# Optimization experiments

Hardware: AMD Instinct MI355X
Metric: run time of the kernel (lower is better)

Reference implementation:

```python
import jax, jax.numpy as jnp
import numpy as np

B, C, H, W = 2, 128, 64, 64
D_STATE, D_CONV, EXPAND = 16, 4, 2
D_INNER = EXPAND * C
DT_RANK = (C + 15) // 16  # ceil(d_model/16) = 8


def layernorm(x, w, b):
    # WithBias_LayerNorm over last (channel) dim, unbiased=False variance
    mu = jnp.mean(x, axis=-1, keepdims=True)
    var = jnp.mean((x - mu) ** 2, axis=-1, keepdims=True)
    return (x - mu) / jnp.sqrt(var + 1e-5) * w + b


def causal_conv1d_silu(x, w, b):
    # x: (b, d, l); w: (d, k) depthwise; causal pad k-1 on left, then SiLU
    k = w.shape[1]
    out = jax.lax.conv_general_dilated(
        x, w[:, None, :], window_strides=(1,), padding=[(k - 1, 0)],
        dimension_numbers=('NCH', 'OIH', 'NCH'), feature_group_count=w.shape[0])
    return jax.nn.silu(out + b[:, None])


def selective_scan(dA, dBu, Cm):
    # dA, dBu: (b, d, l, n); Cm: (b, n, l) -> y: (b, d, l)
    dA_t = jnp.moveaxis(dA, 2, 0)    # (l, b, d, n)
    dBu_t = jnp.moveaxis(dBu, 2, 0)  # (l, b, d, n)
    C_t = jnp.moveaxis(Cm, 2, 0)     # (l, b, n)

    def step(h, inp):
        a, bu, c = inp
        h = a * h + bu
        y = jnp.einsum('bdn,bn->bd', h, c)
        return h, y

    h0 = jnp.zeros(dA.shape[:2] + (dA.shape[3],), dA.dtype)
    _, ys = jax.lax.scan(step, h0, (dA_t, dBu_t, C_t))
    return jnp.moveaxis(ys, 0, 2)  # (b, d, l)


def mamba_branch(x3, W_in, W_z, conv_w, conv_b, W_x, W_dt, b_dt, A, D, W_out):
    # x3: (b, l, d_model) normalized input
    x = jnp.einsum('bld,ed->bel', x3, W_in)  # (b, d_inner, l)
    z = jnp.einsum('bld,ed->bel', x3, W_z)
    x = causal_conv1d_silu(x, conv_w, conv_b)
    xdbl = jnp.einsum('bdl,ed->bel', x, W_x)  # (b, dt_rank+2n, l)
    dt_low = xdbl[:, :DT_RANK]
    Bm = xdbl[:, DT_RANK:DT_RANK + D_STATE]
    Cm = xdbl[:, DT_RANK + D_STATE:]
    delta = jax.nn.softplus(jnp.einsum('brl,dr->bdl', dt_low, W_dt) + b_dt[:, None])
    dA = jnp.exp(delta[:, :, :, None] * A[None, :, None, :])           # (b,d,l,n)
    dBu = jnp.einsum('bdl,bnl->bdln', delta * x, Bm)                    # (b,d,l,n)
    y = selective_scan(dA, dBu, Cm)
    y = y + D[:, None] * x
    y = y * jax.nn.silu(z)
    return jnp.einsum('bdl,od->blo', y, W_out)  # (b, l, d_model)


def setup_inputs() -> dict:
    key = jax.random.key(0)
    ks = jax.random.split(key, 24)
    rn = lambda k, shp, s: jax.random.normal(k, shp, dtype=jnp.float32) * s
    inp = {}
    inp['pan'] = rn(ks[0], (B, C, H, W), 1.0)
    inp['ms'] = rn(ks[1], (B, C, H, W), 1.0)
    inp['norm_w_pan'] = jnp.ones((C,), jnp.float32)
    inp['norm_b_pan'] = jnp.zeros((C,), jnp.float32)
    inp['norm_w_ms'] = jnp.ones((C,), jnp.float32)
    inp['norm_b_ms'] = jnp.zeros((C,), jnp.float32)
    inp['W_in_pan'] = rn(ks[2], (D_INNER, C), C ** -0.5)
    inp['W_in_ms'] = rn(ks[3], (D_INNER, C), C ** -0.5)
    inp['W_z_pan'] = rn(ks[4], (D_INNER, C), C ** -0.5)
    inp['W_z_ms'] = rn(ks[5], (D_INNER, C), C ** -0.5)
    inp['conv_w_pan'] = rn(ks[6], (D_INNER, D_CONV), D_CONV ** -0.5)
    inp['conv_b_pan'] = rn(ks[7], (D_INNER,), 0.02)
    inp['conv_w_ms'] = rn(ks[8], (D_INNER, D_CONV), D_CONV ** -0.5)
    inp['conv_b_ms'] = rn(ks[9], (D_INNER,), 0.02)
    inp['W_x_pan'] = rn(ks[10], (DT_RANK + 2 * D_STATE, D_INNER), D_INNER ** -0.5)
    inp['W_x_ms'] = rn(ks[11], (DT_RANK + 2 * D_STATE, D_INNER), D_INNER ** -0.5)
    dt_std = DT_RANK ** -0.5
    inp['W_dt_pan'] = jax.random.uniform(ks[12], (D_INNER, DT_RANK), jnp.float32, -dt_std, dt_std)
    inp['W_dt_ms'] = jax.random.uniform(ks[13], (D_INNER, DT_RANK), jnp.float32, -dt_std, dt_std)
    # dt bias init: inverse-softplus of dt ~ logU[1e-3, 1e-1]
    u = np.asarray(jax.random.uniform(ks[14], (D_INNER,)))
    dt = np.exp(u * (np.log(0.1) - np.log(0.001)) + np.log(0.001)).clip(min=1e-4)
    inv_dt = dt + np.log(-np.expm1(-dt))
    inp['b_dt_pan'] = jnp.asarray(inv_dt, jnp.float32)
    inp['b_dt_ms'] = jnp.asarray(inv_dt, jnp.float32)
    inp['A_log'] = jnp.log(jnp.broadcast_to(jnp.arange(1, D_STATE + 1, dtype=jnp.float32), (D_INNER, D_STATE)))
    inp['D_pan'] = jnp.ones((D_INNER,), jnp.float32)
    inp['D_ms'] = jnp.ones((D_INNER,), jnp.float32)
    inp['W_out_pan'] = rn(ks[15], (C, D_INNER), D_INNER ** -0.5)
    inp['W_out_ms'] = rn(ks[16], (C, D_INNER), D_INNER ** -0.5)
    return inp


def reference(pan, ms, norm_w_pan, norm_b_pan, norm_w_ms, norm_b_ms,
              W_in_pan, W_in_ms, W_z_pan, W_z_ms,
              conv_w_pan, conv_b_pan, conv_w_ms, conv_b_ms,
              W_x_pan, W_x_ms, W_dt_pan, W_dt_ms, b_dt_pan, b_dt_ms,
              A_log, D_pan, D_ms, W_out_pan, W_out_ms):
    b, c, h, w = pan.shape
    A = -jnp.exp(A_log)
    pan3 = layernorm(pan.reshape(b, c, h * w).transpose(0, 2, 1), norm_w_pan, norm_b_pan)
    ms3 = layernorm(ms.reshape(b, c, h * w).transpose(0, 2, 1), norm_w_ms, norm_b_ms)
    out_pan = mamba_branch(pan3, W_in_pan, W_z_pan, conv_w_pan, conv_b_pan,
                           W_x_pan, W_dt_pan, b_dt_pan, A, D_pan, W_out_pan)
    out_ms = mamba_branch(ms3, W_in_ms, W_z_ms, conv_w_ms, conv_b_ms,
                          W_x_ms, W_dt_ms, b_dt_ms, A, D_ms, W_out_ms)
    out_pan = out_pan.transpose(0, 2, 1).reshape(b, c, h, w)
    out_ms = out_ms.transpose(0, 2, 1).reshape(b, c, h, w)
    return (out_pan, out_ms)
```

## Files before the change

kernel.cpp:

```cpp
#include <hip/hip_runtime.h>
#include <hip/hip_bf16.h>

constexpr int BB = 2;
constexpr int CC = 128;
constexpr int LL = 4096;
constexpr int DI = 256;
constexpr int DS = 16;
constexpr int DR = 8;
constexpr int DX = 40;
constexpr int NZ = 2 * BB;
constexpr int CH = 8;
constexpr int NCH = LL / CH;
constexpr int SEG = 32;

typedef short bf16x8 __attribute__((ext_vector_type(8)));
typedef float f32x4 __attribute__((ext_vector_type(4)));

__device__ __forceinline__ unsigned short f2bf(float x) {
    __hip_bfloat16 h = __float2bfloat16(x);
    return *(unsigned short*)&h;
}
__device__ __forceinline__ float bflo(unsigned u) { return __uint_as_float(u << 16); }
__device__ __forceinline__ float bfhi(unsigned u) { return __uint_as_float(u & 0xffff0000u); }
__device__ __forceinline__ float fast_rcp(float x) { return __builtin_amdgcn_rcpf(x); }
__device__ __forceinline__ float siluf(float x) { return x * fast_rcp(1.f + __expf(-x)); }
__device__ __forceinline__ float softplusf(float x) {
    const float z = exp2f(x * 1.44269504f);
    return (x > 20.f) ? x : 0.69314718f * log2f(1.f + z);
}

__global__ __launch_bounds__(256) void convert_w_kernel(
    const float* __restrict__ Winp, const float* __restrict__ Winm,
    const float* __restrict__ Wzp, const float* __restrict__ Wzm,
    const float* __restrict__ Woutp, const float* __restrict__ Woutm,
    const float* __restrict__ Wxp, const float* __restrict__ Wxm,
    unsigned short* __restrict__ dst)
{
    const int i = blockIdx.x * 256 + threadIdx.x;
    const float* src; int off;
    if (i < 32768)       { src = Winp;  off = i; }
    else if (i < 65536)  { src = Winm;  off = i - 32768; }
    else if (i < 98304)  { src = Wzp;   off = i - 65536; }
    else if (i < 131072) { src = Wzm;   off = i - 98304; }
    else if (i < 163840) { src = Woutp; off = i - 131072; }
    else if (i < 196608) { src = Woutm; off = i - 163840; }
    else if (i < 206848) { src = Wxp;   off = i - 196608; }
    else                 { src = Wxm;   off = i - 206848; }
    dst[i] = f2bf(src[off]);
}

__global__ __launch_bounds__(256) void layernorm_kernel(
    const float* __restrict__ pan, const float* __restrict__ ms,
    const float* __restrict__ wpan, const float* __restrict__ bpan,
    const float* __restrict__ wms, const float* __restrict__ bms,
    unsigned short* __restrict__ x3b)
{
    const int zi = blockIdx.y;
    const int br = zi >> 1, b = zi & 1;
    const float* inp = br ? ms : pan;
    const float* wp = br ? wms : wpan;
    const float* bp = br ? bms : bpan;
    const int l0 = blockIdx.x * 64;
    const int t = threadIdx.x;
    const int lo = t & 63, c4 = t >> 6;
    const float* base = inp + (size_t)b * CC * LL + l0 + lo;
    float vals[32];
    float s = 0.f, s2 = 0.f;
    #pragma unroll
    for (int i = 0; i < 32; i++) {
        const int c = c4 * 32 + i;
        const float v = base[(size_t)c * LL];
        vals[i] = v; s += v; s2 += v * v;
    }
    __shared__ float red[2][4][64];
    red[0][c4][lo] = s; red[1][c4][lo] = s2;
    __syncthreads();
    const float S  = red[0][0][lo] + red[0][1][lo] + red[0][2][lo] + red[0][3][lo];
    const float S2 = red[1][0][lo] + red[1][1][lo] + red[1][2][lo] + red[1][3][lo];
    const float mu = S * (1.f / CC);
    const float var = S2 * (1.f / CC) - mu * mu;
    const float rstd = rsqrtf(var + 1e-5f);
    unsigned short* out = x3b + (size_t)zi * CC * LL + l0 + lo;
    #pragma unroll
    for (int i = 0; i < 32; i++) {
        const int c = c4 * 32 + i;
        out[(size_t)c * LL] = f2bf((vals[i] - mu) * rstd * wp[c] + bp[c]);
    }
}

__global__ __launch_bounds__(256) void gemm_inz_mfma(
    const unsigned short* __restrict__ wb, const unsigned short* __restrict__ x3b,
    float* __restrict__ xpre, unsigned short* __restrict__ zb16)
{
    const int zi = blockIdx.z;
    const int my = blockIdx.y;
    const unsigned short* W = wb + (my >= 4 ? 65536 : 0) + (zi >= BB ? 32768 : 0);
    const int mbase = (my & 3) * 64;
    const unsigned short* Xb = x3b + (size_t)zi * CC * LL;
    const int n0 = blockIdx.x * 64;
    const int t = threadIdx.x;
    const int w = t >> 6, ln = t & 63;
    const int nf = ln & 15, qb = ln >> 4;
    bf16x8 afrag[4];
    const int mrow = mbase + w * 16 + nf;
    #pragma unroll
    for (int c = 0; c < 4; c++)
        afrag[c] = *(const bf16x8*)(W + (size_t)mrow * CC + c * 32 + qb * 8);
    __shared__ unsigned short Bs[64][40];
    unsigned* Bw = (unsigned*)Bs;
    f32x4 acc[4] = {};
    const int kp = t >> 4, n4 = (t & 15) * 4;
    #pragma unroll
    for (int kc = 0; kc < 4; kc++) {
        const ushort4 a0 = *(const ushort4*)(Xb + (size_t)(kc * 32 + 2 * kp) * LL + n0 + n4);
        const ushort4 a1 = *(const ushort4*)(Xb + (size_t)(kc * 32 + 2 * kp + 1) * LL + n0 + n4);
        if (kc) __syncthreads();
        Bw[(n4 + 0) * 20 + kp] = (unsigned)a0.x | ((unsigned)a1.x << 16);
        Bw[(n4 + 1) * 20 + kp] = (unsigned)a0.y | ((unsigned)a1.y << 16);
        Bw[(n4 + 2) * 20 + kp] = (unsigned)a0.z | ((unsigned)a1.z << 16);
        Bw[(n4 + 3) * 20 + kp] = (unsigned)a0.w | ((unsigned)a1.w << 16);
        __syncthreads();
        #pragma unroll
        for (int ns = 0; ns < 4; ns++) {
            const bf16x8 bf = *(const bf16x8*)(&Bs[ns * 16 + nf][qb * 8]);
            acc[ns] = __builtin_amdgcn_mfma_f32_16x16x32_bf16(afrag[kc], bf, acc[ns], 0, 0, 0);
        }
    }
    if (my >= 4) {
        #pragma unroll
        for (int ns = 0; ns < 4; ns++)
            #pragma unroll
            for (int r = 0; r < 4; r++) {
                const int m = mbase + w * 16 + qb * 4 + r;
                zb16[((size_t)zi * DI + m) * LL + n0 + ns * 16 + nf] = f2bf(acc[ns][r]);
            }
    } else {
        #pragma unroll
        for (int ns = 0; ns < 4; ns++)
            #pragma unroll
            for (int r = 0; r < 4; r++) {
                const int m = mbase + w * 16 + qb * 4 + r;
                xpre[((size_t)zi * DI + m) * LL + n0 + ns * 16 + nf] = acc[ns][r];
            }
    }
}

__global__ __launch_bounds__(256) void conv_silu_kernel(
    const float* __restrict__ xpre,
    const float* __restrict__ cw0, const float* __restrict__ cb0,
    const float* __restrict__ cw1, const float* __restrict__ cb1,
    unsigned short* __restrict__ xc)
{
    const int idx = blockIdx.x * 256 + threadIdx.x;
    const int row = idx >> 9;
    const int l0 = (idx & 511) * CH;
    const int zi = row >> 8, d = row & (DI - 1);
    const float* cw = (zi >= BB) ? cw1 : cw0;
    const float* cb = (zi >= BB) ? cb1 : cb0;
    const float w0 = cw[d * 4 + 0], w1 = cw[d * 4 + 1];
    const float w2 = cw[d * 4 + 2], w3 = cw[d * 4 + 3];
    const float bias = cb[d];
    const float* x_g = xpre + (size_t)row * LL;
    float xv[CH + 3];
    if (l0 > 0) {
        const float4 hm = *(const float4*)(x_g + l0 - 4);
        xv[0] = hm.y; xv[1] = hm.z; xv[2] = hm.w;
    } else { xv[0] = 0.f; xv[1] = 0.f; xv[2] = 0.f; }
    #pragma unroll
    for (int j = 0; j < 2; j++) {
        const float4 v = *(const float4*)(x_g + l0 + 4 * j);
        xv[4 * j + 3] = v.x; xv[4 * j + 4] = v.y;
        xv[4 * j + 5] = v.z; xv[4 * j + 6] = v.w;
    }
    ushort4 r0, r1;
    #pragma unroll
    for (int i = 0; i < CH; i++) {
        const float val = siluf(w0 * xv[i] + w1 * xv[i + 1] + w2 * xv[i + 2] + w3 * xv[i + 3] + bias);
        if (i < 4) ((unsigned short*)&r0)[i] = f2bf(val);
        else       ((unsigned short*)&r1)[i - 4] = f2bf(val);
    }
    unsigned short* out = xc + (size_t)row * LL + l0;
    *(ushort4*)(out + 0) = r0;
    *(ushort4*)(out + 4) = r1;
}

__global__ __launch_bounds__(256) void gemm_x_mfma(
    const unsigned short* __restrict__ wb, const unsigned short* __restrict__ xc,
    unsigned short* __restrict__ xdbl16)
{
    const int zi = blockIdx.z;
    const unsigned short* W = wb + 196608 + (zi >= BB ? 10240 : 0);
    const unsigned short* Xb = xc + (size_t)zi * DI * LL;
    const int n0 = blockIdx.x * 64;
    const int t = threadIdx.x;
    const int w = t >> 6, ln = t & 63;
    const int nf = ln & 15, qb = ln >> 4;
    bf16x8 zfrag;
    #pragma unroll
    for (int j = 0; j < 8; j++) zfrag[j] = 0;
    bf16x8 afrag[8];
    const int mrow = w * 16 + nf;
    #pragma unroll
    for (int c = 0; c < 8; c++)
        afrag[c] = (mrow < DX) ? *(const bf16x8*)(W + (size_t)mrow * DI + c * 32 + qb * 8) : zfrag;
    __shared__ unsigned short Bs[64][40];
    unsigned* Bw = (unsigned*)Bs;
    f32x4 acc[4] = {};
    const int kp = t >> 4, n4 = (t & 15) * 4;
    #pragma unroll
    for (int kc = 0; kc < 8; kc++) {
        const ushort4 a0 = *(const ushort4*)(Xb + (size_t)(kc * 32 + 2 * kp) * LL + n0 + n4);
        const ushort4 a1 = *(const ushort4*)(Xb + (size_t)(kc * 32 + 2 * kp + 1) * LL + n0 + n4);
        if (kc) __syncthreads();
        Bw[(n4 + 0) * 20 + kp] = (unsigned)a0.x | ((unsigned)a1.x << 16);
        Bw[(n4 + 1) * 20 + kp] = (unsigned)a0.y | ((unsigned)a1.y << 16);
        Bw[(n4 + 2) * 20 + kp] = (unsigned)a0.z | ((unsigned)a1.z << 16);
        Bw[(n4 + 3) * 20 + kp] = (unsigned)a0.w | ((unsigned)a1.w << 16);
        __syncthreads();
        #pragma unroll
        for (int ns = 0; ns < 4; ns++) {
            const bf16x8 bf = *(const bf16x8*)(&Bs[ns * 16 + nf][qb * 8]);
            acc[ns] = __builtin_amdgcn_mfma_f32_16x16x32_bf16(afrag[kc], bf, acc[ns], 0, 0, 0);
        }
    }
    #pragma unroll
    for (int ns = 0; ns < 4; ns++)
        #pragma unroll
        for (int r = 0; r < 4; r++) {
            const int m = w * 16 + qb * 4 + r;
            if (m < DX)
                xdbl16[((size_t)zi * DX + m) * LL + n0 + ns * 16 + nf] = f2bf(acc[ns][r]);
        }
}

__global__ __launch_bounds__(256) void gemm_out_mfma(
    const unsigned short* __restrict__ wb, const unsigned short* __restrict__ yb,
    float* __restrict__ outg)
{
    const int zi = blockIdx.z;
    const unsigned short* W = wb + 131072 + (zi >= BB ? 32768 : 0);
    const int mbase = blockIdx.y * 64;
    const unsigned short* Xb = yb + (size_t)zi * DI * LL;
    const int n0 = blockIdx.x * 64;
    const int t = threadIdx.x;
    const int w = t >> 6, ln = t & 63;
    const int nf = ln & 15, qb = ln >> 4;
    bf16x8 afrag[8];
    const int mrow = mbase + w * 16 + nf;
    #pragma unroll
    for (int c = 0; c < 8; c++)
        afrag[c] = *(const bf16x8*)(W + (size_t)mrow * DI + c * 32 + qb * 8);
    __shared__ unsigned short Bs[64][40];
    unsigned* Bw = (unsigned*)Bs;
    f32x4 acc[4] = {};
    const int kp = t >> 4, n4 = (t & 15) * 4;
    #pragma unroll
    for (int kc = 0; kc < 8; kc++) {
        const ushort4 a0 = *(const ushort4*)(Xb + (size_t)(kc * 32 + 2 * kp) * LL + n0 + n4);
        const ushort4 a1 = *(const ushort4*)(Xb + (size_t)(kc * 32 + 2 * kp + 1) * LL + n0 + n4);
        if (kc) __syncthreads();
        Bw[(n4 + 0) * 20 + kp] = (unsigned)a0.x | ((unsigned)a1.x << 16);
        Bw[(n4 + 1) * 20 + kp] = (unsigned)a0.y | ((unsigned)a1.y << 16);
        Bw[(n4 + 2) * 20 + kp] = (unsigned)a0.z | ((unsigned)a1.z << 16);
        Bw[(n4 + 3) * 20 + kp] = (unsigned)a0.w | ((unsigned)a1.w << 16);
        __syncthreads();
        #pragma unroll
        for (int ns = 0; ns < 4; ns++) {
            const bf16x8 bf = *(const bf16x8*)(&Bs[ns * 16 + nf][qb * 8]);
            acc[ns] = __builtin_amdgcn_mfma_f32_16x16x32_bf16(afrag[kc], bf, acc[ns], 0, 0, 0);
        }
    }
    #pragma unroll
    for (int ns = 0; ns < 4; ns++)
        #pragma unroll
        for (int r = 0; r < 4; r++) {
            const int m = mbase + w * 16 + qb * 4 + r;
            outg[((size_t)zi * CC + m) * LL + n0 + ns * 16 + nf] = acc[ns][r];
        }
}

__global__ __launch_bounds__(512, 8) void scan_fused(
    const unsigned short* __restrict__ xc, const unsigned short* __restrict__ xdbl16,
    const float* __restrict__ A_log,
    const float* __restrict__ Wdt0, const float* __restrict__ Wdt1,
    const float* __restrict__ bdt0, const float* __restrict__ bdt1,
    const float* __restrict__ D0, const float* __restrict__ D1,
    const unsigned short* __restrict__ zb16, unsigned short* __restrict__ yb)
{
    const int blk = blockIdx.x;
    const int zi = blk >> 8;
    const int d  = blk & (DI - 1);
    const int t = threadIdx.x;
    const int l0 = t * CH;
    __shared__ float Ssh[DS * (NCH + 1)];
    __shared__ float sdl_sh[NCH];
    __shared__ float Pseg[DS * (SEG + 1)];
    __shared__ float Sseg[DS * (SEG + 1)];
    const unsigned short* xdb = xdbl16 + (size_t)zi * DX * LL;
    const float* Wdt = (zi >= BB) ? Wdt1 : Wdt0;
    const float* bdt = (zi >= BB) ? bdt1 : bdt0;
    const float dbias = bdt[d];
    float rx[CH];
    {
        const uint4 xv4 = *(const uint4*)(xc + (size_t)blk * LL + l0);
        rx[0] = bflo(xv4.x); rx[1] = bfhi(xv4.x);
        rx[2] = bflo(xv4.y); rx[3] = bfhi(xv4.y);
        rx[4] = bflo(xv4.z); rx[5] = bfhi(xv4.z);
        rx[6] = bflo(xv4.w); rx[7] = bfhi(xv4.w);
    }
    float e[CH], rdlx[CH];
    {
        float acc[CH];
        #pragma unroll
        for (int i = 0; i < CH; i++) acc[i] = dbias;
        #pragma unroll
        for (int r = 0; r < DR; r++) {
            const float wr = Wdt[d * DR + r];
            const uint4 v = *(const uint4*)(xdb + (size_t)r * LL + l0);
            acc[0] = fmaf(wr, bflo(v.x), acc[0]); acc[1] = fmaf(wr, bfhi(v.x), acc[1]);
            acc[2] = fmaf(wr, bflo(v.y), acc[2]); acc[3] = fmaf(wr, bfhi(v.y), acc[3]);
            acc[4] = fmaf(wr, bflo(v.z), acc[4]); acc[5] = fmaf(wr, bfhi(v.z), acc[5]);
            acc[6] = fmaf(wr, bflo(v.w), acc[6]); acc[7] = fmaf(wr, bfhi(v.w), acc[7]);
        }
        float sdl = 0.f;
        #pragma unroll
        for (int i = 0; i < CH; i++) {
            const float sp = softplusf(acc[i]);
            sdl += sp;
            rdlx[i] = sp * rx[i];
            e[i] = __expf(-sp);
        }
        sdl_sh[t] = sdl;
    }
    bool fast = true;
    #pragma unroll
    for (int n = 0; n < DS; n++)
        fast = fast && (fabsf(__expf(A_log[d * DS + n]) - (float)(n + 1)) < 1e-3f);
    const unsigned short* Bbase = xdb + (size_t)DR * LL;
    const unsigned short* Cbase = Bbase + (size_t)DS * LL;
    float y[CH];
    const int n2 = t & 15, sg = t >> 4;

    if (fast) {
        float pw[CH];
        #pragma unroll
        for (int i = 0; i < CH; i++) pw[i] = 1.f;
        #pragma unroll 2
        for (int n = 0; n < DS; n++) {
            const uint4 bv = *(const uint4*)(Bbase + (size_t)n * LL + l0);
            float hn = 0.f;
            pw[0] *= e[0]; hn = fmaf(pw[0], hn, rdlx[0] * bflo(bv.x));
            pw[1] *= e[1]; hn = fmaf(pw[1], hn, rdlx[1] * bfhi(bv.x));
            pw[2] *= e[2]; hn = fmaf(pw[2], hn, rdlx[2] * bflo(bv.y));
            pw[3] *= e[3]; hn = fmaf(pw[3], hn, rdlx[3] * bfhi(bv.y));
            pw[4] *= e[4]; hn = fmaf(pw[4], hn, rdlx[4] * bflo(bv.z));
            pw[5] *= e[5]; hn = fmaf(pw[5], hn, rdlx[5] * bfhi(bv.z));
            pw[6] *= e[6]; hn = fmaf(pw[6], hn, rdlx[6] * bflo(bv.w));
            pw[7] *= e[7]; hn = fmaf(pw[7], hn, rdlx[7] * bfhi(bv.w));
            Ssh[n * (NCH + 1) + t] = hn;
        }
        __syncthreads();
        {
            const float Ann = -(float)(n2 + 1);
            float P = 1.f, S = 0.f;
            #pragma unroll
            for (int k = 0; k < 16; k++) {
                const int c = sg * 16 + k;
                const float p = __expf(Ann * sdl_sh[c]);
                const float s = Ssh[n2 * (NCH + 1) + c];
                S = fmaf(p, S, s);
                P *= p;
            }
            Pseg[n2 * (SEG + 1) + sg] = P;
            Sseg[n2 * (SEG + 1) + sg] = S;
        }
        __syncthreads();
        if (t < DS) {
            float h = 0.f;
            #pragma unroll 4
            for (int c2 = 0; c2 < SEG; c2++) {
                const float p = Pseg[t * (SEG + 1) + c2];
                const float s = Sseg[t * (SEG + 1) + c2];
                Sseg[t * (SEG + 1) + c2] = h;
                h = fmaf(p, h, s);
            }
        }
        __syncthreads();
        {
            const float Ann = -(float)(n2 + 1);
            float h = Sseg[n2 * (SEG + 1) + sg];
            #pragma unroll
            for (int k = 0; k < 16; k++) {
                const int c = sg * 16 + k;
                const float p = __expf(Ann * sdl_sh[c]);
                const float s = Ssh[n2 * (NCH + 1) + c];
                Ssh[n2 * (NCH + 1) + c] = h;
                h = fmaf(p, h, s);
            }
        }
        __syncthreads();
        #pragma unroll
        for (int i = 0; i < CH; i++) { y[i] = 0.f; pw[i] = 1.f; }
        #pragma unroll 2
        for (int n = 0; n < DS; n++) {
            const uint4 bv = *(const uint4*)(Bbase + (size_t)n * LL + l0);
            const uint4 cv = *(const uint4*)(Cbase + (size_t)n * LL + l0);
            float hn = Ssh[n * (NCH + 1) + t];
            pw[0] *= e[0]; hn = fmaf(pw[0], hn, rdlx[0] * bflo(bv.x)); y[0] = fmaf(hn, bflo(cv.x), y[0]);
            pw[1] *= e[1]; hn = fmaf(pw[1], hn, rdlx[1] * bfhi(bv.x)); y[1] = fmaf(hn, bfhi(cv.x), y[1]);
            pw[2] *= e[2]; hn = fmaf(pw[2], hn, rdlx[2] * bflo(bv.y)); y[2] = fmaf(hn, bflo(cv.y), y[2]);
            pw[3] *= e[3]; hn = fmaf(pw[3], hn, rdlx[3] * bfhi(bv.y)); y[3] = fmaf(hn, bfhi(cv.y), y[3]);
            pw[4] *= e[4]; hn = fmaf(pw[4], hn, rdlx[4] * bflo(bv.z)); y[4] = fmaf(hn, bflo(cv.z), y[4]);
            pw[5] *= e[5]; hn = fmaf(pw[5], hn, rdlx[5] * bfhi(bv.z)); y[5] = fmaf(hn, bfhi(cv.z), y[5]);
            pw[6] *= e[6]; hn = fmaf(pw[6], hn, rdlx[6] * bflo(bv.w)); y[6] = fmaf(hn, bflo(cv.w), y[6]);
            pw[7] *= e[7]; hn = fmaf(pw[7], hn, rdlx[7] * bfhi(bv.w)); y[7] = fmaf(hn, bfhi(cv.w), y[7]);
        }
    } else {
        float rdl[CH];
        #pragma unroll
        for (int i = 0; i < CH; i++) rdl[i] = -0.69314718f * log2f(e[i]);
        #pragma unroll 2
        for (int n = 0; n < DS; n++) {
            const float An = -__expf(A_log[d * DS + n]);
            const uint4 bv = *(const uint4*)(Bbase + (size_t)n * LL + l0);
            float hn = 0.f;
            hn = fmaf(__expf(rdl[0] * An), hn, rdlx[0] * bflo(bv.x));
            hn = fmaf(__expf(rdl[1] * An), hn, rdlx[1] * bfhi(bv.x));
            hn = fmaf(__expf(rdl[2] * An), hn, rdlx[2] * bflo(bv.y));
            hn = fmaf(__expf(rdl[3] * An), hn, rdlx[3] * bfhi(bv.y));
            hn = fmaf(__expf(rdl[4] * An), hn, rdlx[4] * bflo(bv.z));
            hn = fmaf(__expf(rdl[5] * An), hn, rdlx[5] * bfhi(bv.z));
            hn = fmaf(__expf(rdl[6] * An), hn, rdlx[6] * bflo(bv.w));
            hn = fmaf(__expf(rdl[7] * An), hn, rdlx[7] * bfhi(bv.w));
            Ssh[n * (NCH + 1) + t] = hn;
        }
        __syncthreads();
        {
            const float Ann = -__expf(A_log[d * DS + n2]);
            float P = 1.f, S = 0.f;
            #pragma unroll
            for (int k = 0; k < 16; k++) {
                const int c = sg * 16 + k;
                const float p = __expf(Ann * sdl_sh[c]);
                const float s = Ssh[n2 * (NCH + 1) + c];
                S = fmaf(p, S, s);
                P *= p;
            }
            Pseg[n2 * (SEG + 1) + sg] = P;
            Sseg[n2 * (SEG + 1) + sg] = S;
        }
        __syncthreads();
        if (t < DS) {
            float h = 0.f;
            #pragma unroll 4
            for (int c2 = 0; c2 < SEG; c2++) {
                const float p = Pseg[t * (SEG + 1) + c2];
                const float s = Sseg[t * (SEG + 1) + c2];
                Sseg[t * (SEG + 1) + c2] = h;
                h = fmaf(p, h, s);
            }
        }
        __syncthreads();
        {
            const float Ann = -__expf(A_log[d * DS + n2]);
            float h = Sseg[n2 * (SEG + 1) + sg];
            #pragma unroll
            for (int k = 0; k < 16; k++) {
                const int c = sg * 16 + k;
                const float p = __expf(Ann * sdl_sh[c]);
                const float s = Ssh[n2 * (NCH + 1) + c];
                Ssh[n2 * (NCH + 1) + c] = h;
                h = fmaf(p, h, s);
            }
        }
        __syncthreads();
        #pragma unroll
        for (int i = 0; i < CH; i++) y[i] = 0.f;
        #pragma unroll 2
        for (int n = 0; n < DS; n++) {
            const float An = -__expf(A_log[d * DS + n]);
            const uint4 bv = *(const uint4*)(Bbase + (size_t)n * LL + l0);
            const uint4 cv = *(const uint4*)(Cbase + (size_t)n * LL + l0);
            float hn = Ssh[n * (NCH + 1) + t];
            hn = fmaf(__expf(rdl[0] * An), hn, rdlx[0] * bflo(bv.x)); y[0] = fmaf(hn, bflo(cv.x), y[0]);
            hn = fmaf(__expf(rdl[1] * An), hn, rdlx[1] * bfhi(bv.x)); y[1] = fmaf(hn, bfhi(cv.x), y[1]);
            hn = fmaf(__expf(rdl[2] * An), hn, rdlx[2] * bflo(bv.y)); y[2] = fmaf(hn, bflo(cv.y), y[2]);
            hn = fmaf(__expf(rdl[3] * An), hn, rdlx[3] * bfhi(bv.y)); y[3] = fmaf(hn, bfhi(cv.y), y[3]);
            hn = fmaf(__expf(rdl[4] * An), hn, rdlx[4] * bflo(cv.z)); y[4] = fmaf(hn, bflo(cv.z), y[4]);
            hn = fmaf(__expf(rdl[5] * An), hn, rdlx[5] * bfhi(bv.z)); y[5] = fmaf(hn, bfhi(cv.z), y[5]);
            hn = fmaf(__expf(rdl[6] * An), hn, rdlx[6] * bflo(bv.w)); y[6] = fmaf(hn, bflo(cv.w), y[6]);
            hn = fmaf(__expf(rdl[7] * An), hn, rdlx[7] * bfhi(bv.w)); y[7] = fmaf(hn, bfhi(cv.w), y[7]);
        }
    }
    const float Dd = ((zi >= BB) ? D1 : D0)[d];
    const unsigned short* z_g = zb16 + (size_t)blk * LL + l0;
    unsigned short* y_g = yb + (size_t)blk * LL + l0;
    {
        const uint4 zv = *(const uint4*)z_g;
        float zf[CH];
        zf[0] = bflo(zv.x); zf[1] = bfhi(zv.x); zf[2] = bflo(zv.y); zf[3] = bfhi(zv.y);
        zf[4] = bflo(zv.z); zf[5] = bfhi(zv.z); zf[6] = bflo(zv.w); zf[7] = bfhi(zv.w);
        ushort4 r0, r1;
        #pragma unroll
        for (int i = 0; i < CH; i++) {
            const float val = (y[i] + Dd * rx[i]) * siluf(zf[i]);
            if (i < 4) ((unsigned short*)&r0)[i] = f2bf(val);
            else       ((unsigned short*)&r1)[i - 4] = f2bf(val);
        }
        *(ushort4*)(y_g + 0) = r0;
        *(ushort4*)(y_g + 4) = r1;
    }
}

extern "C" void kernel_launch(void* const* d_in, const int* in_sizes, int n_in,
                              void* d_out, int out_size, void* d_ws, size_t ws_size,
                              hipStream_t stream)
{
    (void)in_sizes; (void)n_in; (void)out_size; (void)ws_size;
    auto fp = [&](int i) { return (const float*)d_in[i]; };
    const float *pan = fp(0), *ms = fp(1);
    const float *nwp = fp(2), *nbp = fp(3), *nwm = fp(4), *nbm = fp(5);
    const float *Winp = fp(6), *Winm = fp(7), *Wzp = fp(8), *Wzm = fp(9);
    const float *cwp = fp(10), *cbp = fp(11), *cwm = fp(12), *cbm = fp(13);
    const float *Wxp = fp(14), *Wxm = fp(15);
    const float *Wdtp = fp(16), *Wdtm = fp(17), *bdtp = fp(18), *bdtm = fp(19);
    const float *Alog = fp(20), *Dp = fp(21), *Dm = fp(22);
    const float *Woutp = fp(23), *Woutm = fp(24);

    float* ws = (float*)d_ws;
    unsigned short* x3b = (unsigned short*)ws;
    float* xpre = ws + (size_t)NZ * CC * LL / 2;
    unsigned short* zb16 = (unsigned short*)(xpre + (size_t)NZ * DI * LL);
    unsigned short* xdbl16 = zb16 + (size_t)NZ * DI * LL;
    unsigned short* yb = xdbl16 + (size_t)NZ * DX * LL;
    unsigned short* wb = yb + (size_t)NZ * DI * LL;
    unsigned short* xc = wb + 217088;
    float* out = (float*)d_out;

    convert_w_kernel<<<dim3(848), 256, 0, stream>>>(Winp, Winm, Wzp, Wzm, Woutp, Woutm, Wxp, Wxm, wb);
    layernorm_kernel<<<dim3(LL / 64, NZ), 256, 0, stream>>>(pan, ms, nwp, nbp, nwm, nbm, x3b);
    gemm_inz_mfma<<<dim3(LL / 64, 8, NZ), 256, 0, stream>>>(wb, x3b, xpre, zb16);
    conv_silu_kernel<<<dim3(NZ * DI * (LL / CH) / 256), 256, 0, stream>>>(xpre, cwp, cbp, cwm, cbm, xc);
    gemm_x_mfma<<<dim3(LL / 64, 1, NZ), 256, 0, stream>>>(wb, xc, xdbl16);
    scan_fused<<<dim3(NZ * DI), 512, 0, stream>>>(xc, xdbl16, Alog, Wdtp, Wdtm, bdtp, bdtm,
                                                  Dp, Dm, zb16, yb);
    gemm_out_mfma<<<dim3(LL / 64, 2, NZ), 256, 0, stream>>>(wb, yb, out);
}
```

Measured before the change: 172.2 us.

## Fuse layernorm with weight conversion and conv+SiLU into x-projection GEMM

Merges the weight-conversion and layernorm kernels into one launch and folds the causal depthwise conv plus SiLU into the x-projection GEMM's operand staging. The in-projection result is now stored as bf16 instead of fp32, halving that intermediate's traffic and dropping a separate conv kernel pass. It also raises the unroll in a scan loop and fixes a wrong operand (cv.z instead of bv.z) in the scan recurrence. The bf16 intermediate adds rounding before the conv, and the fused GEMM reloads neighbouring elements for the conv halo.

```diff
diff --git a/kernel.cpp b/kernel.cpp
--- a/kernel.cpp
+++ b/kernel.cpp
@@ -22,6 +22,7 @@
 }
 __device__ __forceinline__ float bflo(unsigned u) { return __uint_as_float(u << 16); }
 __device__ __forceinline__ float bfhi(unsigned u) { return __uint_as_float(u & 0xffff0000u); }
+__device__ __forceinline__ float bfu(unsigned short u) { return __uint_as_float((unsigned)u << 16); }
 __device__ __forceinline__ float fast_rcp(float x) { return __builtin_amdgcn_rcpf(x); }
 __device__ __forceinline__ float siluf(float x) { return x * fast_rcp(1.f + __expf(-x)); }
 __device__ __forceinline__ float softplusf(float x) {
@@ -29,39 +30,38 @@
     return (x > 20.f) ? x : 0.69314718f * log2f(1.f + z);
 }
 
-__global__ __launch_bounds__(256) void convert_w_kernel(
+__global__ __launch_bounds__(256) void prep_kernel(
+    const float* __restrict__ pan, const float* __restrict__ ms,
+    const float* __restrict__ wpan, const float* __restrict__ bpan,
+    const float* __restrict__ wms, const float* __restrict__ bms,
     const float* __restrict__ Winp, const float* __restrict__ Winm,
     const float* __restrict__ Wzp, const float* __restrict__ Wzm,
     const float* __restrict__ Woutp, const float* __restrict__ Woutm,
     const float* __restrict__ Wxp, const float* __restrict__ Wxm,
-    unsigned short* __restrict__ dst)
+    unsigned short* __restrict__ x3b, unsigned short* __restrict__ wb)
 {
-    const int i = blockIdx.x * 256 + threadIdx.x;
-    const float* src; int off;
-    if (i < 32768)       { src = Winp;  off = i; }
-    else if (i < 65536)  { src = Winm;  off = i - 32768; }
-    else if (i < 98304)  { src = Wzp;   off = i - 65536; }
-    else if (i < 131072) { src = Wzm;   off = i - 98304; }
-    else if (i < 163840) { src = Woutp; off = i - 131072; }
-    else if (i < 196608) { src = Woutm; off = i - 163840; }
-    else if (i < 206848) { src = Wxp;   off = i - 196608; }
-    else                 { src = Wxm;   off = i - 206848; }
-    dst[i] = f2bf(src[off]);
-}
-
-__global__ __launch_bounds__(256) void layernorm_kernel(
-    const float* __restrict__ pan, const float* __restrict__ ms,
-    const float* __restrict__ wpan, const float* __restrict__ bpan,
-    const float* __restrict__ wms, const float* __restrict__ bms,
-    unsigned short* __restrict__ x3b)
-{
-    const int zi = blockIdx.y;
+    const int bx = blockIdx.x;
+    const int t = threadIdx.x;
+    if (bx >= 256) {
+        const int i = (bx - 256) * 256 + t;
+        const float* src; int off;
+        if (i < 32768)       { src = Winp;  off = i; }
+        else if (i < 65536)  { src = Winm;  off = i - 32768; }
+        else if (i < 98304)  { src = Wzp;   off = i - 65536; }
+        else if (i < 131072) { src = Wzm;   off = i - 98304; }
+        else if (i < 163840) { src = Woutp; off = i - 131072; }
+        else if (i < 196608) { src = Woutm; off = i - 163840; }
+        else if (i < 206848) { src = Wxp;   off = i - 196608; }
+        else                 { src = Wxm;   off = i - 206848; }
+        wb[i] = f2bf(src[off]);
+        return;
+    }
+    const int zi = bx >> 6;
     const int br = zi >> 1, b = zi & 1;
     const float* inp = br ? ms : pan;
     const float* wp = br ? wms : wpan;
     const float* bp = br ? bms : bpan;
-    const int l0 = blockIdx.x * 64;
-    const int t = threadIdx.x;
+    const int l0 = (bx & 63) * 64;
     const int lo = t & 63, c4 = t >> 6;
     const float* base = inp + (size_t)b * CC * LL + l0 + lo;
     float vals[32];
@@ -90,7 +90,7 @@
 
 __global__ __launch_bounds__(256) void gemm_inz_mfma(
     const unsigned short* __restrict__ wb, const unsigned short* __restrict__ x3b,
-    float* __restrict__ xpre, unsigned short* __restrict__ zb16)
+    unsigned short* __restrict__ xpre16, unsigned short* __restrict__ zb16)
 {
     const int zi = blockIdx.z;
     const int my = blockIdx.y;
@@ -126,71 +126,28 @@
             acc[ns] = __builtin_amdgcn_mfma_f32_16x16x32_bf16(afrag[kc], bf, acc[ns], 0, 0, 0);
         }
     }
-    if (my >= 4) {
-        #pragma unroll
-        for (int ns = 0; ns < 4; ns++)
-            #pragma unroll
-            for (int r = 0; r < 4; r++) {
-                const int m = mbase + w * 16 + qb * 4 + r;
-                zb16[((size_t)zi * DI + m) * LL + n0 + ns * 16 + nf] = f2bf(acc[ns][r]);
-            }
-    } else {
-        #pragma unroll
-        for (int ns = 0; ns < 4; ns++)
-            #pragma unroll
-            for (int r = 0; r < 4; r++) {
-                const int m = mbase + w * 16 + qb * 4 + r;
-                xpre[((size_t)zi * DI + m) * LL + n0 + ns * 16 + nf] = acc[ns][r];
-            }
-    }
-}
-
-__global__ __launch_bounds__(256) void conv_silu_kernel(
-    const float* __restrict__ xpre,
+    unsigned short* dst = (my >= 4) ? zb16 : xpre16;
+    #pragma unroll
+    for (int ns = 0; ns < 4; ns++)
+        #pragma unroll
+        for (int r = 0; r < 4; r++) {
+            const int m = mbase + w * 16 + qb * 4 + r;
+            dst[((size_t)zi * DI + m) * LL + n0 + ns * 16 + nf] = f2bf(acc[ns][r]);
+        }
+}
+
+__global__ __launch_bounds__(256) void gemm_x_mfma(
+    const unsigned short* __restrict__ wb, const unsigned short* __restrict__ xpre16,
     const float* __restrict__ cw0, const float* __restrict__ cb0,
     const float* __restrict__ cw1, const float* __restrict__ cb1,
-    unsigned short* __restrict__ xc)
-{
-    const int idx = blockIdx.x * 256 + threadIdx.x;
-    const int row = idx >> 9;
-    const int l0 = (idx & 511) * CH;
-    const int zi = row >> 8, d = row & (DI - 1);
-    const float* cw = (zi >= BB) ? cw1 : cw0;
-    const float* cb = (zi >= BB) ? cb1 : cb0;
-    const float w0 = cw[d * 4 + 0], w1 = cw[d * 4 + 1];
-    const float w2 = cw[d * 4 + 2], w3 = cw[d * 4 + 3];
-    const float bias = cb[d];
-    const float* x_g = xpre + (size_t)row * LL;
-    float xv[CH + 3];
-    if (l0 > 0) {
-        const float4 hm = *(const float4*)(x_g + l0 - 4);
-        xv[0] = hm.y; xv[1] = hm.z; xv[2] = hm.w;
-    } else { xv[0] = 0.f; xv[1] = 0.f; xv[2] = 0.f; }
-    #pragma unroll
-    for (int j = 0; j < 2; j++) {
-        const float4 v = *(const float4*)(x_g + l0 + 4 * j);
-        xv[4 * j + 3] = v.x; xv[4 * j + 4] = v.y;
-        xv[4 * j + 5] = v.z; xv[4 * j + 6] = v.w;
-    }
-    ushort4 r0, r1;
-    #pragma unroll
-    for (int i = 0; i < CH; i++) {
-        const float val = siluf(w0 * xv[i] + w1 * xv[i + 1] + w2 * xv[i + 2] + w3 * xv[i + 3] + bias);
-        if (i < 4) ((unsigned short*)&r0)[i] = f2bf(val);
-        else       ((unsigned short*)&r1)[i - 4] = f2bf(val);
-    }
-    unsigned short* out = xc + (size_t)row * LL + l0;
-    *(ushort4*)(out + 0) = r0;
-    *(ushort4*)(out + 4) = r1;
-}
-
-__global__ __launch_bounds__(256) void gemm_x_mfma(
-    const unsigned short* __restrict__ wb, const unsigned short* __restrict__ xc,
-    unsigned short* __restrict__ xdbl16)
+    unsigned short* __restrict__ xc, unsigned short* __restrict__ xdbl16)
 {
     const int zi = blockIdx.z;
     const unsigned short* W = wb + 196608 + (zi >= BB ? 10240 : 0);
-    const unsigned short* Xb = xc + (size_t)zi * DI * LL;
+    const float* cw = (zi >= BB) ? cw1 : cw0;
+    const float* cb = (zi >= BB) ? cb1 : cb0;
+    const unsigned short* Xb = xpre16 + (size_t)zi * DI * LL;
+    unsigned short* xcb = xc + (size_t)zi * DI * LL;
     const int n0 = blockIdx.x * 64;
     const int t = threadIdx.x;
     const int w = t >> 6, ln = t & 63;
@@ -209,13 +166,35 @@
     const int kp = t >> 4, n4 = (t & 15) * 4;
     #pragma unroll
     for (int kc = 0; kc < 8; kc++) {
-        const ushort4 a0 = *(const ushort4*)(Xb + (size_t)(kc * 32 + 2 * kp) * LL + n0 + n4);
-        const ushort4 a1 = *(const ushort4*)(Xb + (size_t)(kc * 32 + 2 * kp + 1) * LL + n0 + n4);
+        ushort4 o[2];
+        #pragma unroll
+        for (int rr = 0; rr < 2; rr++) {
+            const int e = kc * 32 + 2 * kp + rr;
+            const unsigned short* xp = Xb + (size_t)e * LL + n0 + n4;
+            const ushort4 cur = *(const ushort4*)xp;
+            float xm1, xm2, xm3;
+            if (n0 + n4 == 0) { xm1 = 0.f; xm2 = 0.f; xm3 = 0.f; }
+            else {
+                const ushort4 prev = *(const ushort4*)(xp - 4);
+                xm3 = bfu(prev.y); xm2 = bfu(prev.z); xm1 = bfu(prev.w);
+            }
+            const float c0 = bfu(cur.x), c1 = bfu(cur.y);
+            const float c2 = bfu(cur.z), c3 = bfu(cur.w);
+            const float w0 = cw[e * 4 + 0], w1 = cw[e * 4 + 1];
+            const float w2 = cw[e * 4 + 2], w3 = cw[e * 4 + 3];
+            const float bias = cb[e];
+            o[rr].x = f2bf(siluf(w0 * xm3 + w1 * xm2 + w2 * xm1 + w3 * c0 + bias));
+            o[rr].y = f2bf(siluf(w0 * xm2 + w1 * xm1 + w2 * c0 + w3 * c1 + bias));
+            o[rr].z = f2bf(siluf(w0 * xm1 + w1 * c0 + w2 * c1 + w3 * c2 + bias));
+            o[rr].w = f2bf(siluf(w0 * c0 + w1 * c1 + w2 * c2 + w3 * c3 + bias));
+        }
+        *(ushort4*)(xcb + (size_t)(kc * 32 + 2 * kp) * LL + n0 + n4) = o[0];
+        *(ushort4*)(xcb + (size_t)(kc * 32 + 2 * kp + 1) * LL + n0 + n4) = o[1];
         if (kc) __syncthreads();
-        Bw[(n4 + 0) * 20 + kp] = (unsigned)a0.x | ((unsigned)a1.x << 16);
-        Bw[(n4 + 1) * 20 + kp] = (unsigned)a0.y | ((unsigned)a1.y << 16);
-        Bw[(n4 + 2) * 20 + kp] = (unsigned)a0.z | ((unsigned)a1.z << 16);
-        Bw[(n4 + 3) * 20 + kp] = (unsigned)a0.w | ((unsigned)a1.w << 16);
+        Bw[(n4 + 0) * 20 + kp] = (unsigned)(unsigned short)o[0].x | ((unsigned)(unsigned short)o[1].x << 16);
+        Bw[(n4 + 1) * 20 + kp] = (unsigned)(unsigned short)o[0].y | ((unsigned)(unsigned short)o[1].y << 16);
+        Bw[(n4 + 2) * 20 + kp] = (unsigned)(unsigned short)o[0].z | ((unsigned)(unsigned short)o[1].z << 16);
+        Bw[(n4 + 3) * 20 + kp] = (unsigned)(unsigned short)o[0].w | ((unsigned)(unsigned short)o[1].w << 16);
         __syncthreads();
         #pragma unroll
         for (int ns = 0; ns < 4; ns++) {
@@ -345,7 +324,7 @@
         float pw[CH];
         #pragma unroll
         for (int i = 0; i < CH; i++) pw[i] = 1.f;
-        #pragma unroll 2
+        #pragma unroll 4
         for (int n = 0; n < DS; n++) {
             const uint4 bv = *(const uint4*)(Bbase + (size_t)n * LL + l0);
             float hn = 0.f;
@@ -486,7 +465,7 @@
             hn = fmaf(__expf(rdl[1] * An), hn, rdlx[1] * bfhi(bv.x)); y[1] = fmaf(hn, bfhi(cv.x), y[1]);
             hn = fmaf(__expf(rdl[2] * An), hn, rdlx[2] * bflo(bv.y)); y[2] = fmaf(hn, bflo(cv.y), y[2]);
             hn = fmaf(__expf(rdl[3] * An), hn, rdlx[3] * bfhi(bv.y)); y[3] = fmaf(hn, bfhi(cv.y), y[3]);
-            hn = fmaf(__expf(rdl[4] * An), hn, rdlx[4] * bflo(cv.z)); y[4] = fmaf(hn, bflo(cv.z), y[4]);
+            hn = fmaf(__expf(rdl[4] * An), hn, rdlx[4] * bflo(bv.z)); y[4] = fmaf(hn, bflo(cv.z), y[4]);
             hn = fmaf(__expf(rdl[5] * An), hn, rdlx[5] * bfhi(bv.z)); y[5] = fmaf(hn, bfhi(cv.z), y[5]);
             hn = fmaf(__expf(rdl[6] * An), hn, rdlx[6] * bflo(bv.w)); y[6] = fmaf(hn, bflo(cv.w), y[6]);
             hn = fmaf(__expf(rdl[7] * An), hn, rdlx[7] * bfhi(bv.w)); y[7] = fmaf(hn, bfhi(cv.w), y[7]);
@@ -527,21 +506,21 @@
     const float *Alog = fp(20), *Dp = fp(21), *Dm = fp(22);
     const float *Woutp = fp(23), *Woutm = fp(24);
 
-    float* ws = (float*)d_ws;
-    unsigned short* x3b = (unsigned short*)ws;
-    float* xpre = ws + (size_t)NZ * CC * LL / 2;
-    unsigned short* zb16 = (unsigned short*)(xpre + (size_t)NZ * DI * LL);
-    unsigned short* xdbl16 = zb16 + (size_t)NZ * DI * LL;
-    unsigned short* yb = xdbl16 + (size_t)NZ * DX * LL;
-    unsigned short* wb = yb + (size_t)NZ * DI * LL;
-    unsigned short* xc = wb + 217088;
+    unsigned short* us = (unsigned short*)d_ws;
+    unsigned short* x3b    = us;
+    unsigned short* xpre16 = x3b    + (size_t)NZ * CC * LL;
+    unsigned short* zb16   = xpre16 + (size_t)NZ * DI * LL;
+    unsigned short* xdbl16 = zb16   + (size_t)NZ * DI * LL;
+    unsigned short* yb     = xdbl16 + (size_t)NZ * DX * LL;
+    unsigned short* xc     = yb     + (size_t)NZ * DI * LL;
+    unsigned short* wb     = xc     + (size_t)NZ * DI * LL;
     float* out = (float*)d_out;
 
-    convert_w_kernel<<<dim3(848), 256, 0, stream>>>(Winp, Winm, Wzp, Wzm, Woutp, Woutm, Wxp, Wxm, wb);
-    layernorm_kernel<<<dim3(LL / 64, NZ), 256, 0, stream>>>(pan, ms, nwp, nbp, nwm, nbm, x3b);
-    gemm_inz_mfma<<<dim3(LL / 64, 8, NZ), 256, 0, stream>>>(wb, x3b, xpre, zb16);
-    conv_silu_kernel<<<dim3(NZ * DI * (LL / CH) / 256), 256, 0, stream>>>(xpre, cwp, cbp, cwm, cbm, xc);
-    gemm_x_mfma<<<dim3(LL / 64, 1, NZ), 256, 0, stream>>>(wb, xc, xdbl16);
+    prep_kernel<<<dim3(256 + 848), 256, 0, stream>>>(
+        pan, ms, nwp, nbp, nwm, nbm,
+        Winp, Winm, Wzp, Wzm, Woutp, Woutm, Wxp, Wxm, x3b, wb);
+    gemm_inz_mfma<<<dim3(LL / 64, 8, NZ), 256, 0, stream>>>(wb, x3b, xpre16, zb16);
+    gemm_x_mfma<<<dim3(LL / 64, 1, NZ), 256, 0, stream>>>(wb, xpre16, cwp, cbp, cwm, cbm, xc, xdbl16);
     scan_fused<<<dim3(NZ * DI), 512, 0, stream>>>(xc, xdbl16, Alog, Wdtp, Wdtm, bdtp, bdtm,
                                                   Dp, Dm, zb16, yb);
     gemm_out_mfma<<<dim3(LL / 64, 2, NZ), 256, 0, stream>>>(wb, yb, out);
```

After: 170.6 us. About the same (-0.9%).
